# Kernel tuning notes

Measured on AMD Instinct MI355X. Metric: run time of the kernel, lower is better.

Reference implementation:

```python
import jax, jax.numpy as jnp
import numpy as np

N_NODES = 30000
N_EDGES = 300000
NUM_GRAPHS = 512
HID = 600
IN_FEATS = 9
NUM_TASKS = 128


def setup_inputs() -> dict:
    key = jax.random.key(0)
    ks = jax.random.split(key, 20)
    s = 0.05  # small init scale to keep activations bounded over 5 layers
    inp = {
        'x': jax.random.normal(ks[0], (N_NODES, IN_FEATS), jnp.float32),
        'edge_index': jax.random.randint(ks[1], (2, N_EDGES), 0, N_NODES, jnp.int64),
        'batch_ind': jnp.sort(jax.random.randint(ks[2], (N_NODES,), 0, NUM_GRAPHS, jnp.int64)),
        'w1_0': jax.random.normal(ks[3], (IN_FEATS, HID), jnp.float32) * s,
        'b1_0': jax.random.normal(ks[4], (HID,), jnp.float32) * s,
        'w2_0': jax.random.normal(ks[5], (HID, HID), jnp.float32) * s,
        'b2_0': jax.random.normal(ks[6], (HID,), jnp.float32) * s,
        'w1_r': jax.random.normal(ks[7], (4, HID, HID), jnp.float32) * s,
        'b1_r': jax.random.normal(ks[8], (4, HID), jnp.float32) * s,
        'w2_r': jax.random.normal(ks[9], (4, HID, HID), jnp.float32) * s,
        'b2_r': jax.random.normal(ks[10], (4, HID), jnp.float32) * s,
        'cw1': jax.random.normal(ks[11], (HID, 256), jnp.float32) * s,
        'cb1': jax.random.normal(ks[12], (256,), jnp.float32) * s,
        'cw2': jax.random.normal(ks[13], (256, 256), jnp.float32) * s,
        'cb2': jax.random.normal(ks[14], (256,), jnp.float32) * s,
        'cw3': jax.random.normal(ks[15], (256, NUM_TASKS), jnp.float32) * s,
        'cb3': jax.random.normal(ks[16], (NUM_TASKS,), jnp.float32) * s,
    }
    return inp


def _gin_conv(h, edge_index, w1, b1, w2, b2):
    # sum-aggregate neighbor features: messages flow src -> dst
    msgs = h[edge_index[0]]                                   # [E, d] gather
    agg = jax.ops.segment_sum(msgs, edge_index[1], num_segments=N_NODES)
    z = h + agg                                               # (1 + eps) * x + agg, eps = 0
    z = jax.nn.relu(z @ w1 + b1) @ w2 + b2                    # per-layer MLP [in, 600, 600]
    return z


def _forward(x, edge_index, batch_ind, w1_0, b1_0, w2_0, b2_0,
             w1_r, b1_r, w2_r, b2_r, cw1, cb1, cw2, cb2, cw3, cb3):
    h = _gin_conv(x, edge_index, w1_0, b1_0, w2_0, b2_0)
    h = jax.nn.relu(h)  # inter-layer activation (dropout is identity in eval)
    for i in range(4):  # layers 1..4 (fixed, structurally distinct params)
        h = _gin_conv(h, edge_index, w1_r[i], b1_r[i], w2_r[i], b2_r[i])
        if i < 3:
            h = jax.nn.relu(h)  # no act/dropout after final GNN layer (jk=None)
    feats = jax.ops.segment_sum(h, batch_ind, num_segments=NUM_GRAPHS)  # global_add_pool
    z = jax.nn.relu(feats @ cw1 + cb1)
    z = jax.nn.relu(z @ cw2 + cb2)
    return z @ cw3 + cb3  # [NUM_GRAPHS, NUM_TASKS]


def reference(x, edge_index, batch_ind, w1_0, b1_0, w2_0, b2_0,
              w1_r, b1_r, w2_r, b2_r, cw1, cb1, cw2, cb2, cw3, cb3):
    return _forward(x, edge_index, batch_ind, w1_0, b1_0, w2_0, b2_0,
                    w1_r, b1_r, w2_r, b2_r, cw1, cb1, cw2, cb2, cw3, cb3)
```

## Files before the change

kernel.cpp:

```cpp
#include <hip/hip_runtime.h>

#define N_NODES 30000
#define N_EDGES 300000
#define NUM_GRAPHS 512
#define HID 600
#define IN_FEATS 9
#define NUM_TASKS 128

#define MPAD 30080
#define HPAD 640
#define K0PAD 32

typedef __attribute__((ext_vector_type(4))) float f32x4;
typedef __attribute__((ext_vector_type(8))) short bf16x8;


__device__ __forceinline__ float bflo(unsigned int v) {
  union { unsigned int u; float f; } c; c.u = v << 16; return c.f;
}
__device__ __forceinline__ float bfhi(unsigned int v) {
  union { unsigned int u; float f; } c; c.u = v & 0xffff0000u; return c.f;
}
__device__ __forceinline__ unsigned short f2bf(float f) {
  union { float f; unsigned int u; } c; c.f = f;
  unsigned int u = c.u;
  return (unsigned short)((u + 0x7fffu + ((u >> 16) & 1u)) >> 16);
}
__device__ __forceinline__ unsigned int pack2(float a, float b) {
  return (unsigned int)f2bf(a) | ((unsigned int)f2bf(b) << 16);
}


__global__ void k_hist(const int* __restrict__ keys, int* __restrict__ counts, int n) {
  int i = blockIdx.x * blockDim.x + threadIdx.x;
  if (i < n) atomicAdd(&counts[keys[i]], 1);
}

__global__ __launch_bounds__(1024) void k_exscan(const int* __restrict__ in,
                                                 int* __restrict__ out, int n) {
  __shared__ int buf[1024];
  int tid = threadIdx.x;
  int CH = (n + 1023) / 1024;
  int base = tid * CH;
  int s = 0;
  for (int j = 0; j < CH; ++j) {
    int i = base + j;
    if (i < n) s += in[i];
  }
  buf[tid] = s;
  __syncthreads();
  for (int off = 1; off < 1024; off <<= 1) {
    int t = (tid >= off) ? buf[tid - off] : 0;
    __syncthreads();
    buf[tid] += t;
    __syncthreads();
  }
  int pre = (tid == 0) ? 0 : buf[tid - 1];
  for (int j = 0; j < CH; ++j) {
    int i = base + j;
    if (i <= n) out[i] = pre;
    if (i < n) pre += in[i];
  }
}

__global__ void k_copy_int(const int* __restrict__ in, int* __restrict__ out, int n) {
  int i = blockIdx.x * blockDim.x + threadIdx.x;
  if (i < n) out[i] = in[i];
}

__global__ void k_scatter(const int* __restrict__ src, const int* __restrict__ dst,
                          int* __restrict__ cursor, int* __restrict__ edge_src, int E) {
  int e = blockIdx.x * blockDim.x + threadIdx.x;
  if (e < E) {
    int pos = atomicAdd(&cursor[dst[e]], 1);
    edge_src[pos] = src[e];
  }
}


__global__ void k_wt_all(const float* __restrict__ w1_0, const float* __restrict__ w2_0,
                         const float* __restrict__ w1_r, const float* __restrict__ w2_r,
                         unsigned short* __restrict__ wt0, unsigned short* __restrict__ wts) {
  int idx = blockIdx.x * 256 + threadIdx.x;
  const int S0 = HPAD * K0PAD;
  const int SW = HPAD * HPAD;
  if (idx < S0) {
    int n = idx / K0PAD, k = idx % K0PAD;
    float v = (n < HID && k < IN_FEATS) ? w1_0[(size_t)k * HID + n] : 0.f;
    wt0[idx] = f2bf(v);
    return;
  }
  idx -= S0;
  if (idx >= 9 * SW) return;
  int w = idx / SW, r = idx % SW;
  int n = r / HPAD, k = r % HPAD;
  const float* W;
  if (w == 0) W = w2_0;
  else if (w < 5) W = w1_r + (size_t)(w - 1) * HID * HID;
  else W = w2_r + (size_t)(w - 5) * HID * HID;
  float v = (n < HID && k < HID) ? W[(size_t)k * HID + n] : 0.f;
  wts[(size_t)w * SW + r] = f2bf(v);
}

__global__ void k_bias_all(const float* __restrict__ b1_0, const float* __restrict__ b2_0,
                           const float* __restrict__ b1_r, const float* __restrict__ b2_r,
                           float* __restrict__ biases) {
  int idx = blockIdx.x * 256 + threadIdx.x;
  if (idx >= 10 * HPAD) return;
  int w = idx / HPAD, i = idx % HPAD;
  float v = 0.f;
  if (i < HID) {
    if (w == 0) v = b1_0[i];
    else if (w == 1) v = b2_0[i];
    else if (w < 6) v = b1_r[(size_t)(w - 2) * HID + i];
    else v = b2_r[(size_t)(w - 6) * HID + i];
  }
  biases[idx] = v;
}

__global__ void k_xconv(const float* __restrict__ x, unsigned short* __restrict__ xb) {
  int idx = blockIdx.x * 256 + threadIdx.x;
  if (idx >= MPAD * K0PAD) return;
  int m = idx >> 5, k = idx & 31;
  float v = (m < N_NODES && k < IN_FEATS) ? x[(size_t)m * IN_FEATS + k] : 0.f;
  xb[idx] = f2bf(v);
}


template <int U>
__global__ __launch_bounds__(256) void k_agg_bf16(
    const unsigned int* __restrict__ h, const int* __restrict__ ptr,
    const int* __restrict__ esrc, unsigned int* __restrict__ z, int n_nodes) {
  int wave = threadIdx.x >> 6, lane = threadIdx.x & 63;
  int node = blockIdx.x * 4 + wave;
  if (node >= n_nodes) return;
  int beg = ptr[node], end = ptr[node + 1];
  const unsigned int* hn = h + (size_t)node * U;
  float a0[5], a1[5];
#pragma unroll
  for (int i = 0; i < 5; ++i) {
    int u = lane + i * 64;
    if (u < U) { unsigned int v = hn[u]; a0[i] = bflo(v); a1[i] = bfhi(v); }
    else { a0[i] = 0.f; a1[i] = 0.f; }
  }
  int e = beg;
  for (; e + 2 <= end; e += 2) {
    const unsigned int* p0 = h + (size_t)esrc[e] * U;
    const unsigned int* p1 = h + (size_t)esrc[e + 1] * U;
    unsigned int v0[5], v1[5];
#pragma unroll
    for (int i = 0; i < 5; ++i) {
      int u = lane + i * 64;
      if (u < U) { v0[i] = p0[u]; v1[i] = p1[u]; }
      else { v0[i] = 0; v1[i] = 0; }
    }
#pragma unroll
    for (int i = 0; i < 5; ++i) {
      a0[i] += bflo(v0[i]) + bflo(v1[i]);
      a1[i] += bfhi(v0[i]) + bfhi(v1[i]);
    }
  }
  if (e < end) {
    const unsigned int* p0 = h + (size_t)esrc[e] * U;
#pragma unroll
    for (int i = 0; i < 5; ++i) {
      int u = lane + i * 64;
      if (u < U) { unsigned int v = p0[u]; a0[i] += bflo(v); a1[i] += bfhi(v); }
    }
  }
  unsigned int* zn = z + (size_t)node * U;
#pragma unroll
  for (int i = 0; i < 5; ++i) {
    int u = lane + i * 64;
    if (u < U) zn[u] = pack2(a0[i], a1[i]);
  }
}


__global__ __launch_bounds__(256) void k_pool_bf16(
    const unsigned int* __restrict__ h, const int* __restrict__ gptr,
    float* __restrict__ feats) {
  const int U = HPAD / 2;
  __shared__ float red[4][HPAD];
  int t = threadIdx.x;
  int wave = t >> 6, lane = t & 63;
  int g = blockIdx.x;
  int beg = gptr[g], end = gptr[g + 1];
  float a0[5] = {0.f, 0.f, 0.f, 0.f, 0.f}, a1[5] = {0.f, 0.f, 0.f, 0.f, 0.f};
  for (int i = beg + wave; i < end; i += 4) {
    const unsigned int* hi = h + (size_t)i * U;
#pragma unroll
    for (int j = 0; j < 5; ++j) {
      unsigned int v = hi[lane + j * 64];
      a0[j] += bflo(v); a1[j] += bfhi(v);
    }
  }
#pragma unroll
  for (int j = 0; j < 5; ++j) {
    int u = lane + j * 64;
    red[wave][2 * u] = a0[j];
    red[wave][2 * u + 1] = a1[j];
  }
  __syncthreads();
  float* fg = feats + (size_t)g * HPAD;
  for (int c = t; c < HPAD; c += 256)
    fg[c] = red[0][c] + red[1][c] + red[2][c] + red[3][c];
}


__global__ __launch_bounds__(256) void k_mgemm(
    const unsigned short* __restrict__ A, const unsigned short* __restrict__ Bt,
    const float* __restrict__ bias, unsigned short* __restrict__ C,
    int lda, int ldb, int ldc, int K, int relu, int gy) {
  int G = gridDim.x;
  int orig = blockIdx.x;
  int q = G >> 3, r = G & 7;
  int xcd = orig & 7, local = orig >> 3;
  int wgid = (xcd < r ? xcd * (q + 1) : r * (q + 1) + (xcd - r) * q) + local;
  int n0 = (wgid % gy) * 128;
  int m0 = (wgid / gy) * 128;

  __shared__ unsigned short As[128 * 32];
  __shared__ unsigned short Bs[128 * 32];
  int t = threadIdx.x;
  int lane = t & 63, wave = t >> 6;
  int wm = (wave >> 1) * 64, wn = (wave & 1) * 64;

  f32x4 acc[4][4] = {};

  int off0 = t * 8, off1 = t * 8 + 2048;
  int rm0 = off0 >> 5, rk0 = off0 & 31;
  int rm1 = off1 >> 5, rk1 = off1 & 31;

  for (int k0 = 0; k0 < K; k0 += 32) {
    __builtin_amdgcn_global_load_lds(
        (const __attribute__((address_space(1))) unsigned int*)(A + (size_t)(m0 + rm0) * lda + k0 + rk0),
        (__attribute__((address_space(3))) unsigned int*)(As + off0), 16, 0, 0);
    __builtin_amdgcn_global_load_lds(
        (const __attribute__((address_space(1))) unsigned int*)(A + (size_t)(m0 + rm1) * lda + k0 + rk1),
        (__attribute__((address_space(3))) unsigned int*)(As + off1), 16, 0, 0);
    __builtin_amdgcn_global_load_lds(
        (const __attribute__((address_space(1))) unsigned int*)(Bt + (size_t)(n0 + rm0) * ldb + k0 + rk0),
        (__attribute__((address_space(3))) unsigned int*)(Bs + off0), 16, 0, 0);
    __builtin_amdgcn_global_load_lds(
        (const __attribute__((address_space(1))) unsigned int*)(Bt + (size_t)(n0 + rm1) * ldb + k0 + rk1),
        (__attribute__((address_space(3))) unsigned int*)(Bs + off1), 16, 0, 0);
    __syncthreads();

    int kk = (lane >> 4) * 8;
    int ra = wm + (lane & 15);
    int rb = wn + (lane & 15);
    bf16x8 a[4], b[4];
#pragma unroll
    for (int i = 0; i < 4; ++i)
      a[i] = *(const bf16x8*)(As + (ra + i * 16) * 32 + kk);
#pragma unroll
    for (int j = 0; j < 4; ++j)
      b[j] = *(const bf16x8*)(Bs + (rb + j * 16) * 32 + kk);
#pragma unroll
    for (int i = 0; i < 4; ++i)
#pragma unroll
      for (int j = 0; j < 4; ++j)
        acc[i][j] = __builtin_amdgcn_mfma_f32_16x16x32_bf16(a[i], b[j], acc[i][j], 0, 0, 0);
    __syncthreads();
  }

  int col = lane & 15, r4 = (lane >> 4) * 4;
#pragma unroll
  for (int j = 0; j < 4; ++j) {
    int n = n0 + wn + j * 16 + col;
    float bv = bias[n];
#pragma unroll
    for (int i = 0; i < 4; ++i) {
      int mb = m0 + wm + i * 16 + r4;
#pragma unroll
      for (int rr = 0; rr < 4; ++rr) {
        float v = acc[i][j][rr] + bv;
        if (relu) v = fmaxf(v, 0.f);
        C[(size_t)(mb + rr) * ldc + n] = f2bf(v);
      }
    }
  }
}


__global__ __launch_bounds__(256) void k_classifier(
    const float* __restrict__ feats,
    const float* __restrict__ cw1, const float* __restrict__ cb1,
    const float* __restrict__ cw2, const float* __restrict__ cb2,
    const float* __restrict__ cw3, const float* __restrict__ cb3,
    float* __restrict__ out) {
  __shared__ float f[HID];
  __shared__ float red[4][256];
  __shared__ float z1[256];
  __shared__ float z2[256];
  int g = blockIdx.x;
  int t = threadIdx.x;
  int wave = t >> 6, lane = t & 63;
  for (int i = t; i < HID; i += 256) f[i] = feats[(size_t)g * HPAD + i];
  __syncthreads();

  {
    float acc[4] = {0.f, 0.f, 0.f, 0.f};
    int k0 = wave * 150, k1 = k0 + 150;
    for (int k = k0; k < k1; ++k) {
      float fv = f[k];
      const float* row = cw1 + (size_t)k * 256;
#pragma unroll
      for (int j = 0; j < 4; ++j) acc[j] += fv * row[lane + j * 64];
    }
#pragma unroll
    for (int j = 0; j < 4; ++j) red[wave][lane + j * 64] = acc[j];
  }
  __syncthreads();
  z1[t] = fmaxf(red[0][t] + red[1][t] + red[2][t] + red[3][t] + cb1[t], 0.f);
  __syncthreads();

  {
    float acc[4] = {0.f, 0.f, 0.f, 0.f};
    int k0 = wave * 64, k1 = k0 + 64;
    for (int k = k0; k < k1; ++k) {
      float zv = z1[k];
      const float* row = cw2 + (size_t)k * 256;
#pragma unroll
      for (int j = 0; j < 4; ++j) acc[j] += zv * row[lane + j * 64];
    }
    __syncthreads();
#pragma unroll
    for (int j = 0; j < 4; ++j) red[wave][lane + j * 64] = acc[j];
  }
  __syncthreads();
  z2[t] = fmaxf(red[0][t] + red[1][t] + red[2][t] + red[3][t] + cb2[t], 0.f);
  __syncthreads();

  {
    float a0 = 0.f, a1 = 0.f;
    int k0 = wave * 64, k1 = k0 + 64;
    for (int k = k0; k < k1; ++k) {
      float zv = z2[k];
      const float* row = cw3 + (size_t)k * NUM_TASKS;
      a0 += zv * row[lane];
      a1 += zv * row[lane + 64];
    }
    __syncthreads();
    red[wave][lane] = a0;
    red[wave][lane + 64] = a1;
  }
  __syncthreads();
  if (t < NUM_TASKS)
    out[(size_t)g * NUM_TASKS + t] = red[0][t] + red[1][t] + red[2][t] + red[3][t] + cb3[t];
}


extern "C" void kernel_launch(void* const* d_in, const int* in_sizes, int n_in,
                              void* d_out, int out_size, void* d_ws, size_t ws_size,
                              hipStream_t stream) {
  const float* x      = (const float*)d_in[0];
  const int*   ei     = (const int*)d_in[1];
  const int*   batch  = (const int*)d_in[2];
  const float* w1_0   = (const float*)d_in[3];
  const float* b1_0   = (const float*)d_in[4];
  const float* w2_0   = (const float*)d_in[5];
  const float* b2_0   = (const float*)d_in[6];
  const float* w1_r   = (const float*)d_in[7];
  const float* b1_r   = (const float*)d_in[8];
  const float* w2_r   = (const float*)d_in[9];
  const float* b2_r   = (const float*)d_in[10];
  const float* cw1    = (const float*)d_in[11];
  const float* cb1    = (const float*)d_in[12];
  const float* cw2    = (const float*)d_in[13];
  const float* cb2    = (const float*)d_in[14];
  const float* cw3    = (const float*)d_in[15];
  const float* cb3    = (const float*)d_in[16];
  float* out = (float*)d_out;

  const int* e_src = ei;
  const int* e_dst = ei + N_EDGES;

  const size_t HBUF = (size_t)MPAD * HPAD;
  const size_t ZBUF = (size_t)MPAD * K0PAD;
  const size_t WT   = (size_t)HPAD * HPAD;

  unsigned short* hA  = (unsigned short*)d_ws;
  unsigned short* hB  = hA + HBUF;
  unsigned short* hC  = hB + HBUF;
  unsigned short* z0  = hC + HBUF;
  unsigned short* xb  = z0 + ZBUF;
  unsigned short* wt0 = xb + ZBUF;
  unsigned short* wts = wt0 + (size_t)HPAD * K0PAD;
  float* biases = (float*)(wts + 9 * WT);
  float* feats  = biases + 10 * HPAD;
  int* row_ptr  = (int*)(feats + (size_t)NUM_GRAPHS * HPAD);
  int* counts   = row_ptr + (N_NODES + 1);
  int* edge_src = counts + N_NODES;
  int* gptr     = edge_src + N_EDGES;
  int* gcnt     = gptr + (NUM_GRAPHS + 1);

  {
    int total = HPAD * K0PAD + 9 * HPAD * HPAD;
    k_wt_all<<<(total + 255) / 256, 256, 0, stream>>>(w1_0, w2_0, w1_r, w2_r, wt0, wts);
  }
  k_bias_all<<<(10 * HPAD + 255) / 256, 256, 0, stream>>>(b1_0, b2_0, b1_r, b2_r, biases);
  k_xconv<<<(MPAD * K0PAD + 255) / 256, 256, 0, stream>>>(x, xb);

  hipMemsetAsync(counts, 0, N_NODES * sizeof(int), stream);
  k_hist<<<(N_EDGES + 255) / 256, 256, 0, stream>>>(e_dst, counts, N_EDGES);
  k_exscan<<<1, 1024, 0, stream>>>(counts, row_ptr, N_NODES);
  k_copy_int<<<(N_NODES + 255) / 256, 256, 0, stream>>>(row_ptr, counts, N_NODES);
  k_scatter<<<(N_EDGES + 255) / 256, 256, 0, stream>>>(e_src, e_dst, counts, edge_src, N_EDGES);

  hipMemsetAsync(gcnt, 0, NUM_GRAPHS * sizeof(int), stream);
  k_hist<<<(N_NODES + 255) / 256, 256, 0, stream>>>(batch, gcnt, N_NODES);
  k_exscan<<<1, 1024, 0, stream>>>(gcnt, gptr, NUM_GRAPHS);

  const int G = (MPAD / 128) * (HPAD / 128);
  const int GY = HPAD / 128;

  k_agg_bf16<K0PAD / 2><<<(N_NODES + 3) / 4, 256, 0, stream>>>(
      (const unsigned int*)xb, row_ptr, edge_src, (unsigned int*)z0, N_NODES);
  k_mgemm<<<G, 256, 0, stream>>>(z0, wt0, biases + 0 * HPAD, hC, K0PAD, K0PAD, HPAD, K0PAD, 1, GY);
  k_mgemm<<<G, 256, 0, stream>>>(hC, wts, biases + 1 * HPAD, hA, HPAD, HPAD, HPAD, HPAD, 1, GY);

  unsigned short* h = hA;
  unsigned short* z = hB;
  unsigned short* tb = hC;
  for (int i = 0; i < 4; ++i) {
    k_agg_bf16<HPAD / 2><<<(N_NODES + 3) / 4, 256, 0, stream>>>(
        (const unsigned int*)h, row_ptr, edge_src, (unsigned int*)z, N_NODES);
    k_mgemm<<<G, 256, 0, stream>>>(z, wts + (1 + (size_t)i) * WT, biases + (2 + i) * HPAD, tb,
                                   HPAD, HPAD, HPAD, HPAD, 1, GY);
    k_mgemm<<<G, 256, 0, stream>>>(tb, wts + (5 + (size_t)i) * WT, biases + (6 + i) * HPAD, z,
                                   HPAD, HPAD, HPAD, HPAD, (i < 3) ? 1 : 0, GY);
    unsigned short* tmp = h; h = z; z = tmp;
  }

  k_pool_bf16<<<NUM_GRAPHS, 256, 0, stream>>>((const unsigned int*)h, gptr, feats);
  k_classifier<<<NUM_GRAPHS, 256, 0, stream>>>(feats, cw1, cb1, cw2, cb2, cw3, cb3, out);
}
```

Baseline: 823.2 us.

## Tile weight transpose, add feature-sliced aggregation, process K=64 per GEMM iteration

Replaces the strided per-element weight transpose with an LDS-tiled transpose kernel so both global reads and writes are coalesced. Adds a column-sliced aggregation kernel that gives each node's 32-word slice to half a wave, and uses it for two of the four hidden layers, apparently as an A/B experiment. The GEMM now loads two 32-wide K chunks into separate LDS buffers before each barrier, halving the number of syncs per tile at the cost of doubled LDS use. Mixing two aggregation kernels across layers adds complexity, and the sliced kernel hardcodes a grid that relies on N_NODES being a multiple of 8.

```diff
diff --git a/kernel.cpp b/kernel.cpp
--- a/kernel.cpp
+++ b/kernel.cpp
@@ -78,28 +78,44 @@
 }
 
 
-__global__ void k_wt_all(const float* __restrict__ w1_0, const float* __restrict__ w2_0,
-                         const float* __restrict__ w1_r, const float* __restrict__ w2_r,
-                         unsigned short* __restrict__ wt0, unsigned short* __restrict__ wts) {
+__global__ void k_wt0(const float* __restrict__ w1_0, unsigned short* __restrict__ wt0) {
   int idx = blockIdx.x * 256 + threadIdx.x;
-  const int S0 = HPAD * K0PAD;
-  const int SW = HPAD * HPAD;
-  if (idx < S0) {
-    int n = idx / K0PAD, k = idx % K0PAD;
-    float v = (n < HID && k < IN_FEATS) ? w1_0[(size_t)k * HID + n] : 0.f;
-    wt0[idx] = f2bf(v);
-    return;
-  }
-  idx -= S0;
-  if (idx >= 9 * SW) return;
-  int w = idx / SW, r = idx % SW;
-  int n = r / HPAD, k = r % HPAD;
+  if (idx >= HPAD * K0PAD) return;
+  int n = idx / K0PAD, k = idx % K0PAD;
+  float v = (n < HID && k < IN_FEATS) ? w1_0[(size_t)k * HID + n] : 0.f;
+  wt0[idx] = f2bf(v);
+}
+
+__global__ __launch_bounds__(256) void k_wt_tiled(
+    const float* __restrict__ w2_0, const float* __restrict__ w1_r,
+    const float* __restrict__ w2_r, unsigned short* __restrict__ wts) {
+  __shared__ float tile[64][65];
+  int b = blockIdx.x;
+  int w = b / 100;
+  int tb = b % 100;
+  int tn = (tb % 10) * 64;
+  int tk = (tb / 10) * 64;
   const float* W;
   if (w == 0) W = w2_0;
   else if (w < 5) W = w1_r + (size_t)(w - 1) * HID * HID;
   else W = w2_r + (size_t)(w - 5) * HID * HID;
-  float v = (n < HID && k < HID) ? W[(size_t)k * HID + n] : 0.f;
-  wts[(size_t)w * SW + r] = f2bf(v);
+  int t = threadIdx.x;
+  int lx = t & 63, ly = t >> 6;
+#pragma unroll
+  for (int i = 0; i < 16; ++i) {
+    int k = tk + ly + i * 4;
+    int n = tn + lx;
+    float v = (k < HID && n < HID) ? W[(size_t)k * HID + n] : 0.f;
+    tile[ly + i * 4][lx] = v;
+  }
+  __syncthreads();
+  unsigned short* dst = wts + (size_t)w * HPAD * HPAD;
+#pragma unroll
+  for (int i = 0; i < 16; ++i) {
+    int n = tn + ly + i * 4;
+    int k = tk + lx;
+    dst[(size_t)n * HPAD + k] = f2bf(tile[lx][ly + i * 4]);
+  }
 }
 
 __global__ void k_bias_all(const float* __restrict__ b1_0, const float* __restrict__ b2_0,
@@ -177,6 +193,38 @@
 }
 
 
+__global__ __launch_bounds__(256) void k_agg_sliced(
+    const unsigned int* __restrict__ h, const int* __restrict__ ptr,
+    const int* __restrict__ esrc, unsigned int* __restrict__ z) {
+  const int U = HPAD / 2;
+  const int SL = 32;
+  int b = blockIdx.x;
+  int slice = b / (N_NODES / 8);
+  int nb = b % (N_NODES / 8);
+  int t = threadIdx.x;
+  int wave = t >> 6, lane = t & 63;
+  int half = lane >> 5, sub = lane & 31;
+  int node = nb * 8 + wave * 2 + half;
+  int beg = ptr[node], end = ptr[node + 1];
+  const unsigned int* hb = h + (size_t)slice * SL + sub;
+  unsigned int v = hb[(size_t)node * U];
+  float a0 = bflo(v), a1 = bfhi(v);
+  int e = beg;
+  for (; e + 2 <= end; e += 2) {
+    int s0 = esrc[e], s1 = esrc[e + 1];
+    unsigned int v0 = hb[(size_t)s0 * U];
+    unsigned int v1 = hb[(size_t)s1 * U];
+    a0 += bflo(v0) + bflo(v1);
+    a1 += bfhi(v0) + bfhi(v1);
+  }
+  if (e < end) {
+    unsigned int v0 = hb[(size_t)esrc[e] * U];
+    a0 += bflo(v0); a1 += bfhi(v0);
+  }
+  z[(size_t)node * U + slice * SL + sub] = pack2(a0, a1);
+}
+
+
 __global__ __launch_bounds__(256) void k_pool_bf16(
     const unsigned int* __restrict__ h, const int* __restrict__ gptr,
     float* __restrict__ feats) {
@@ -220,8 +268,8 @@
   int n0 = (wgid % gy) * 128;
   int m0 = (wgid / gy) * 128;
 
-  __shared__ unsigned short As[128 * 32];
-  __shared__ unsigned short Bs[128 * 32];
+  __shared__ unsigned short As[2][128 * 32];
+  __shared__ unsigned short Bs[2][128 * 32];
   int t = threadIdx.x;
   int lane = t & 63, wave = t >> 6;
   int wm = (wave >> 1) * 64, wn = (wave & 1) * 64;
@@ -232,36 +280,68 @@
   int rm0 = off0 >> 5, rk0 = off0 & 31;
   int rm1 = off1 >> 5, rk1 = off1 & 31;
 
-  for (int k0 = 0; k0 < K; k0 += 32) {
+  for (int k0 = 0; k0 < K; k0 += 64) {
     __builtin_amdgcn_global_load_lds(
         (const __attribute__((address_space(1))) unsigned int*)(A + (size_t)(m0 + rm0) * lda + k0 + rk0),
-        (__attribute__((address_space(3))) unsigned int*)(As + off0), 16, 0, 0);
+        (__attribute__((address_space(3))) unsigned int*)(&As[0][off0]), 16, 0, 0);
     __builtin_amdgcn_global_load_lds(
         (const __attribute__((address_space(1))) unsigned int*)(A + (size_t)(m0 + rm1) * lda + k0 + rk1),
-        (__attribute__((address_space(3))) unsigned int*)(As + off1), 16, 0, 0);
+        (__attribute__((address_space(3))) unsigned int*)(&As[0][off1]), 16, 0, 0);
     __builtin_amdgcn_global_load_lds(
         (const __attribute__((address_space(1))) unsigned int*)(Bt + (size_t)(n0 + rm0) * ldb + k0 + rk0),
-        (__attribute__((address_space(3))) unsigned int*)(Bs + off0), 16, 0, 0);
+        (__attribute__((address_space(3))) unsigned int*)(&Bs[0][off0]), 16, 0, 0);
     __builtin_amdgcn_global_load_lds(
         (const __attribute__((address_space(1))) unsigned int*)(Bt + (size_t)(n0 + rm1) * ldb + k0 + rk1),
-        (__attribute__((address_space(3))) unsigned int*)(Bs + off1), 16, 0, 0);
+        (__attribute__((address_space(3))) unsigned int*)(&Bs[0][off1]), 16, 0, 0);
+    bool second = (k0 + 32 < K);
+    if (second) {
+      int k1 = k0 + 32;
+      __builtin_amdgcn_global_load_lds(
+          (const __attribute__((address_space(1))) unsigned int*)(A + (size_t)(m0 + rm0) * lda + k1 + rk0),
+          (__attribute__((address_space(3))) unsigned int*)(&As[1][off0]), 16, 0, 0);
+      __builtin_amdgcn_global_load_lds(
+          (const __attribute__((address_space(1))) unsigned int*)(A + (size_t)(m0 + rm1) * lda + k1 + rk1),
+          (__attribute__((address_space(3))) unsigned int*)(&As[1][off1]), 16, 0, 0);
+      __builtin_amdgcn_global_load_lds(
+          (const __attribute__((address_space(1))) unsigned int*)(Bt + (size_t)(n0 + rm0) * ldb + k1 + rk0),
+          (__attribute__((address_space(3))) unsigned int*)(&Bs[1][off0]), 16, 0, 0);
+      __builtin_amdgcn_global_load_lds(
+          (const __attribute__((address_space(1))) unsigned int*)(Bt + (size_t)(n0 + rm1) * ldb + k1 + rk1),
+          (__attribute__((address_space(3))) unsigned int*)(&Bs[1][off1]), 16, 0, 0);
+    }
     __syncthreads();
 
     int kk = (lane >> 4) * 8;
     int ra = wm + (lane & 15);
     int rb = wn + (lane & 15);
-    bf16x8 a[4], b[4];
-#pragma unroll
-    for (int i = 0; i < 4; ++i)
-      a[i] = *(const bf16x8*)(As + (ra + i * 16) * 32 + kk);
-#pragma unroll
-    for (int j = 0; j < 4; ++j)
-      b[j] = *(const bf16x8*)(Bs + (rb + j * 16) * 32 + kk);
-#pragma unroll
-    for (int i = 0; i < 4; ++i)
+    {
+      bf16x8 a[4], bb[4];
+#pragma unroll
+      for (int i = 0; i < 4; ++i)
+        a[i] = *(const bf16x8*)(&As[0][(ra + i * 16) * 32 + kk]);
 #pragma unroll
       for (int j = 0; j < 4; ++j)
-        acc[i][j] = __builtin_amdgcn_mfma_f32_16x16x32_bf16(a[i], b[j], acc[i][j], 0, 0, 0);
+        bb[j] = *(const bf16x8*)(&Bs[0][(rb + j * 16) * 32 + kk]);
+#pragma unroll
+      for (int i = 0; i < 4; ++i)
+#pragma unroll
+        for (int j = 0; j < 4; ++j)
+          acc[i][j] = __builtin_amdgcn_mfma_f32_16x16x32_bf16(a[i], bb[j], acc[i][j], 0, 0, 0);
+    }
+    if (second) {
+      bf16x8 a[4], bb[4];
+#pragma unroll
+      for (int i = 0; i < 4; ++i)
+        a[i] = *(const bf16x8*)(&As[1][(ra + i * 16) * 32 + kk]);
+#pragma unroll
+      for (int j = 0; j < 4; ++j)
+        bb[j] = *(const bf16x8*)(&Bs[1][(rb + j * 16) * 32 + kk]);
+#pragma unroll
+      for (int i = 0; i < 4; ++i)
+#pragma unroll
+        for (int j = 0; j < 4; ++j)
+          acc[i][j] = __builtin_amdgcn_mfma_f32_16x16x32_bf16(a[i], bb[j], acc[i][j], 0, 0, 0);
+    }
     __syncthreads();
   }
 
@@ -396,10 +476,8 @@
   int* gptr     = edge_src + N_EDGES;
   int* gcnt     = gptr + (NUM_GRAPHS + 1);
 
-  {
-    int total = HPAD * K0PAD + 9 * HPAD * HPAD;
-    k_wt_all<<<(total + 255) / 256, 256, 0, stream>>>(w1_0, w2_0, w1_r, w2_r, wt0, wts);
-  }
+  k_wt0<<<(HPAD * K0PAD + 255) / 256, 256, 0, stream>>>(w1_0, wt0);
+  k_wt_tiled<<<9 * 100, 256, 0, stream>>>(w2_0, w1_r, w2_r, wts);
   k_bias_all<<<(10 * HPAD + 255) / 256, 256, 0, stream>>>(b1_0, b2_0, b1_r, b2_r, biases);
   k_xconv<<<(MPAD * K0PAD + 255) / 256, 256, 0, stream>>>(x, xb);
 
@@ -425,8 +503,13 @@
   unsigned short* z = hB;
   unsigned short* tb = hC;
   for (int i = 0; i < 4; ++i) {
-    k_agg_bf16<HPAD / 2><<<(N_NODES + 3) / 4, 256, 0, stream>>>(
-        (const unsigned int*)h, row_ptr, edge_src, (unsigned int*)z, N_NODES);
+    if (i == 0 || i == 2) {
+      k_agg_sliced<<<10 * (N_NODES / 8), 256, 0, stream>>>(
+          (const unsigned int*)h, row_ptr, edge_src, (unsigned int*)z);
+    } else {
+      k_agg_bf16<HPAD / 2><<<(N_NODES + 3) / 4, 256, 0, stream>>>(
+          (const unsigned int*)h, row_ptr, edge_src, (unsigned int*)z, N_NODES);
+    }
     k_mgemm<<<G, 256, 0, stream>>>(z, wts + (1 + (size_t)i) * WT, biases + (2 + i) * HPAD, tb,
                                    HPAD, HPAD, HPAD, HPAD, 1, GY);
     k_mgemm<<<G, 256, 0, stream>>>(tb, wts + (5 + (size_t)i) * WT, biases + (6 + i) * HPAD, z,
```

Measured after the change: 947.6 us. +15.1%, slower.

## Double-buffer GEMM LDS tiles, tile weight transpose, fuse scan with cursor copy

Applied to the files above, without the earlier changes.

The GEMM kernel now double-buffers its A/B LDS tiles. It prefetches the next k-slice with global_load_lds while the MFMAs run on the current slice, and keeps a single barrier per iteration. The weight transpose/convert kernel is replaced by a shared-memory tiled transpose, so global reads and writes are coalesced. The exclusive scan also writes the scatter cursor itself, which removes a separate copy kernel. LDS use per block doubles, which may lower occupancy, and the in-place scan writes to its own input array.

```diff
diff --git a/kernel.cpp b/kernel.cpp
--- a/kernel.cpp
+++ b/kernel.cpp
@@ -37,7 +37,8 @@
 }
 
 __global__ __launch_bounds__(1024) void k_exscan(const int* __restrict__ in,
-                                                 int* __restrict__ out, int n) {
+                                                 int* __restrict__ out,
+                                                 int* cursor, int n) {
   __shared__ int buf[1024];
   int tid = threadIdx.x;
   int CH = (n + 1023) / 1024;
@@ -59,13 +60,12 @@
   for (int j = 0; j < CH; ++j) {
     int i = base + j;
     if (i <= n) out[i] = pre;
-    if (i < n) pre += in[i];
-  }
-}
-
-__global__ void k_copy_int(const int* __restrict__ in, int* __restrict__ out, int n) {
-  int i = blockIdx.x * blockDim.x + threadIdx.x;
-  if (i < n) out[i] = in[i];
+    if (i < n) {
+      int v = in[i];
+      if (cursor) cursor[i] = pre;
+      pre += v;
+    }
+  }
 }
 
 __global__ void k_scatter(const int* __restrict__ src, const int* __restrict__ dst,
@@ -78,28 +78,44 @@
 }
 
 
-__global__ void k_wt_all(const float* __restrict__ w1_0, const float* __restrict__ w2_0,
-                         const float* __restrict__ w1_r, const float* __restrict__ w2_r,
-                         unsigned short* __restrict__ wt0, unsigned short* __restrict__ wts) {
+__global__ void k_wt0(const float* __restrict__ w1_0, unsigned short* __restrict__ wt0) {
   int idx = blockIdx.x * 256 + threadIdx.x;
-  const int S0 = HPAD * K0PAD;
-  const int SW = HPAD * HPAD;
-  if (idx < S0) {
-    int n = idx / K0PAD, k = idx % K0PAD;
-    float v = (n < HID && k < IN_FEATS) ? w1_0[(size_t)k * HID + n] : 0.f;
-    wt0[idx] = f2bf(v);
-    return;
-  }
-  idx -= S0;
-  if (idx >= 9 * SW) return;
-  int w = idx / SW, r = idx % SW;
-  int n = r / HPAD, k = r % HPAD;
+  if (idx >= HPAD * K0PAD) return;
+  int n = idx / K0PAD, k = idx % K0PAD;
+  float v = (n < HID && k < IN_FEATS) ? w1_0[(size_t)k * HID + n] : 0.f;
+  wt0[idx] = f2bf(v);
+}
+
+__global__ __launch_bounds__(256) void k_wt_tiled(
+    const float* __restrict__ w2_0, const float* __restrict__ w1_r,
+    const float* __restrict__ w2_r, unsigned short* __restrict__ wts) {
+  __shared__ float tile[64][65];
+  int b = blockIdx.x;
+  int w = b / 100;
+  int tb = b % 100;
+  int tn = (tb % 10) * 64;
+  int tk = (tb / 10) * 64;
   const float* W;
   if (w == 0) W = w2_0;
   else if (w < 5) W = w1_r + (size_t)(w - 1) * HID * HID;
   else W = w2_r + (size_t)(w - 5) * HID * HID;
-  float v = (n < HID && k < HID) ? W[(size_t)k * HID + n] : 0.f;
-  wts[(size_t)w * SW + r] = f2bf(v);
+  int t = threadIdx.x;
+  int lx = t & 63, ly = t >> 6;
+#pragma unroll
+  for (int i = 0; i < 16; ++i) {
+    int k = tk + ly + i * 4;
+    int n = tn + lx;
+    float v = (k < HID && n < HID) ? W[(size_t)k * HID + n] : 0.f;
+    tile[ly + i * 4][lx] = v;
+  }
+  __syncthreads();
+  unsigned short* dst = wts + (size_t)w * HPAD * HPAD;
+#pragma unroll
+  for (int i = 0; i < 16; ++i) {
+    int n = tn + ly + i * 4;
+    int k = tk + lx;
+    dst[(size_t)n * HPAD + k] = f2bf(tile[lx][ly + i * 4]);
+  }
 }
 
 __global__ void k_bias_all(const float* __restrict__ b1_0, const float* __restrict__ b2_0,
@@ -208,6 +224,11 @@
 }
 
 
+#define GLOAD(gptr, lptr)                                                            \
+  __builtin_amdgcn_global_load_lds(                                                  \
+      (const __attribute__((address_space(1))) unsigned int*)(gptr),                 \
+      (__attribute__((address_space(3))) unsigned int*)(lptr), 16, 0, 0)
+
 __global__ __launch_bounds__(256) void k_mgemm(
     const unsigned short* __restrict__ A, const unsigned short* __restrict__ Bt,
     const float* __restrict__ bias, unsigned short* __restrict__ C,
@@ -220,8 +241,8 @@
   int n0 = (wgid % gy) * 128;
   int m0 = (wgid / gy) * 128;
 
-  __shared__ unsigned short As[128 * 32];
-  __shared__ unsigned short Bs[128 * 32];
+  __shared__ unsigned short As[2][128 * 32];
+  __shared__ unsigned short Bs[2][128 * 32];
   int t = threadIdx.x;
   int lane = t & 63, wave = t >> 6;
   int wm = (wave >> 1) * 64, wn = (wave & 1) * 64;
@@ -232,37 +253,47 @@
   int rm0 = off0 >> 5, rk0 = off0 & 31;
   int rm1 = off1 >> 5, rk1 = off1 & 31;
 
-  for (int k0 = 0; k0 < K; k0 += 32) {
-    __builtin_amdgcn_global_load_lds(
-        (const __attribute__((address_space(1))) unsigned int*)(A + (size_t)(m0 + rm0) * lda + k0 + rk0),
-        (__attribute__((address_space(3))) unsigned int*)(As + off0), 16, 0, 0);
-    __builtin_amdgcn_global_load_lds(
-        (const __attribute__((address_space(1))) unsigned int*)(A + (size_t)(m0 + rm1) * lda + k0 + rk1),
-        (__attribute__((address_space(3))) unsigned int*)(As + off1), 16, 0, 0);
-    __builtin_amdgcn_global_load_lds(
-        (const __attribute__((address_space(1))) unsigned int*)(Bt + (size_t)(n0 + rm0) * ldb + k0 + rk0),
-        (__attribute__((address_space(3))) unsigned int*)(Bs + off0), 16, 0, 0);
-    __builtin_amdgcn_global_load_lds(
-        (const __attribute__((address_space(1))) unsigned int*)(Bt + (size_t)(n0 + rm1) * ldb + k0 + rk1),
-        (__attribute__((address_space(3))) unsigned int*)(Bs + off1), 16, 0, 0);
-    __syncthreads();
-
-    int kk = (lane >> 4) * 8;
-    int ra = wm + (lane & 15);
-    int rb = wn + (lane & 15);
+  const unsigned short* Ar0 = A + (size_t)(m0 + rm0) * lda + rk0;
+  const unsigned short* Ar1 = A + (size_t)(m0 + rm1) * lda + rk1;
+  const unsigned short* Br0 = Bt + (size_t)(n0 + rm0) * ldb + rk0;
+  const unsigned short* Br1 = Bt + (size_t)(n0 + rm1) * ldb + rk1;
+
+  GLOAD(Ar0, &As[0][off0]);
+  GLOAD(Ar1, &As[0][off1]);
+  GLOAD(Br0, &Bs[0][off0]);
+  GLOAD(Br1, &Bs[0][off1]);
+  asm volatile("s_waitcnt vmcnt(0)" ::: "memory");
+  __builtin_amdgcn_s_barrier();
+
+  int nt = K >> 5;
+  int cur = 0;
+  int kk = (lane >> 4) * 8;
+  int ra = wm + (lane & 15);
+  int rb = wn + (lane & 15);
+
+  for (int tt = 0; tt < nt; ++tt) {
+    if (tt + 1 < nt) {
+      int k1 = (tt + 1) << 5;
+      GLOAD(Ar0 + k1, &As[cur ^ 1][off0]);
+      GLOAD(Ar1 + k1, &As[cur ^ 1][off1]);
+      GLOAD(Br0 + k1, &Bs[cur ^ 1][off0]);
+      GLOAD(Br1 + k1, &Bs[cur ^ 1][off1]);
+    }
     bf16x8 a[4], b[4];
 #pragma unroll
     for (int i = 0; i < 4; ++i)
-      a[i] = *(const bf16x8*)(As + (ra + i * 16) * 32 + kk);
+      a[i] = *(const bf16x8*)(&As[cur][(ra + i * 16) * 32 + kk]);
 #pragma unroll
     for (int j = 0; j < 4; ++j)
-      b[j] = *(const bf16x8*)(Bs + (rb + j * 16) * 32 + kk);
+      b[j] = *(const bf16x8*)(&Bs[cur][(rb + j * 16) * 32 + kk]);
 #pragma unroll
     for (int i = 0; i < 4; ++i)
 #pragma unroll
       for (int j = 0; j < 4; ++j)
         acc[i][j] = __builtin_amdgcn_mfma_f32_16x16x32_bf16(a[i], b[j], acc[i][j], 0, 0, 0);
-    __syncthreads();
+    asm volatile("s_waitcnt vmcnt(0)" ::: "memory");
+    __builtin_amdgcn_s_barrier();
+    cur ^= 1;
   }
 
   int col = lane & 15, r4 = (lane >> 4) * 4;
@@ -396,22 +427,19 @@
   int* gptr     = edge_src + N_EDGES;
   int* gcnt     = gptr + (NUM_GRAPHS + 1);
 
-  {
-    int total = HPAD * K0PAD + 9 * HPAD * HPAD;
-    k_wt_all<<<(total + 255) / 256, 256, 0, stream>>>(w1_0, w2_0, w1_r, w2_r, wt0, wts);
-  }
+  k_wt0<<<(HPAD * K0PAD + 255) / 256, 256, 0, stream>>>(w1_0, wt0);
+  k_wt_tiled<<<9 * 100, 256, 0, stream>>>(w2_0, w1_r, w2_r, wts);
   k_bias_all<<<(10 * HPAD + 255) / 256, 256, 0, stream>>>(b1_0, b2_0, b1_r, b2_r, biases);
   k_xconv<<<(MPAD * K0PAD + 255) / 256, 256, 0, stream>>>(x, xb);
 
   hipMemsetAsync(counts, 0, N_NODES * sizeof(int), stream);
   k_hist<<<(N_EDGES + 255) / 256, 256, 0, stream>>>(e_dst, counts, N_EDGES);
-  k_exscan<<<1, 1024, 0, stream>>>(counts, row_ptr, N_NODES);
-  k_copy_int<<<(N_NODES + 255) / 256, 256, 0, stream>>>(row_ptr, counts, N_NODES);
+  k_exscan<<<1, 1024, 0, stream>>>(counts, row_ptr, counts, N_NODES);
   k_scatter<<<(N_EDGES + 255) / 256, 256, 0, stream>>>(e_src, e_dst, counts, edge_src, N_EDGES);
 
   hipMemsetAsync(gcnt, 0, NUM_GRAPHS * sizeof(int), stream);
   k_hist<<<(N_NODES + 255) / 256, 256, 0, stream>>>(batch, gcnt, N_NODES);
-  k_exscan<<<1, 1024, 0, stream>>>(gcnt, gptr, NUM_GRAPHS);
+  k_exscan<<<1, 1024, 0, stream>>>(gcnt, gptr, nullptr, NUM_GRAPHS);
 
   const int G = (MPAD / 128) * (HPAD / 128);
   const int GY = HPAD / 128;
```

Measured after the change: 821.1 us. No clear change (-0.3%).
